# Kernel tuning notes

Hardware: AMD Instinct MI355X
Metric: run time of the kernel (lower is better)

## Reference

```python
import jax, jax.numpy as jnp
import numpy as np

B, L, D = 8, 512, 1024
NUM_SPANS = 6144  # L * max_width


def setup_inputs() -> dict:
    key = jax.random.key(0)
    k_h, k_s, k_w, k_b = jax.random.split(key, 4)
    h = jax.random.normal(k_h, (B, L, D), dtype=jnp.float32)
    span_idx = jax.random.randint(k_s, (B, NUM_SPANS, 2), 0, L, dtype=jnp.int64)
    # Linear(hidden, hidden) params (xavier-ish scale)
    lim = float(np.sqrt(6.0 / (D + D)))
    W = jax.random.uniform(k_w, (D, D), dtype=jnp.float32, minval=-lim, maxval=lim)
    b = jnp.zeros((D,), dtype=jnp.float32)
    return {"h": h, "span_idx": span_idx, "W": W, "b": b}


def reference(h, span_idx, W, b):
    # h: [B, L, D]; span_idx: [B, S, 2] with S = L * width
    Bb, Ll, Dd = h.shape
    start = jnp.clip(span_idx[..., 0], 0, Ll - 1)  # [B, S]
    end = jnp.clip(span_idx[..., 1], 0, Ll - 1)    # [B, S]
    valid = start <= end                            # [B, S]
    # prefix sums: cs[i, t] = sum_{u < t} h[i, u]  -> [B, L+1, D]
    cs = jnp.concatenate([jnp.zeros((Bb, 1, Dd), h.dtype), jnp.cumsum(h, axis=1)], axis=1)
    span_sum = (jnp.take_along_axis(cs, (end + 1)[:, :, None], axis=1)
                - jnp.take_along_axis(cs, start[:, :, None], axis=1))  # [B, S, D]
    count = (end - start + 1).astype(h.dtype)[:, :, None]
    span_rep = jnp.where(valid[:, :, None], span_sum / count, 0.0)  # [B, S, D]
    out = jax.nn.relu(jnp.einsum('bsd,ed->bse', span_rep, W) + b)
    return out.reshape(Bb, Ll, -1, Dd)
```

## Files before the change

### kernel.cpp

```cpp
#include <hip/hip_runtime.h>
#include <hip/hip_bf16.h>
#include <stdint.h>

#define B_DIM 8
#define L_DIM 512
#define D_DIM 1024
#define S_DIM 6144
#define M_DIM (B_DIM * S_DIM)
#define NCHUNK 8
#define CHUNK (L_DIM / NCHUNK)
#define CSB (513 * 1024)

typedef __attribute__((ext_vector_type(8))) short short8;
typedef __attribute__((ext_vector_type(4))) float f32x4;
typedef __attribute__((ext_vector_type(8))) unsigned short us8;

__device__ __forceinline__ unsigned short f2bf(float f) {
    unsigned int u = __float_as_uint(f);
    u += 0x7FFFu + ((u >> 16) & 1u);
    return (unsigned short)(u >> 16);
}

__global__ __launch_bounds__(256) void prep_fused(const float* __restrict__ h,
                                                  float* __restrict__ csum,
                                                  const float* __restrict__ W,
                                                  unsigned short* __restrict__ Wbf) {
    if (blockIdx.x < 256) {
        int tid = blockIdx.x * 256 + threadIdx.x;
        int d = tid & 1023;
        int c = (tid >> 10) & 7;
        int b = tid >> 13;
        const float* hp = h + ((size_t)b * L_DIM + c * CHUNK) * D_DIM + d;
        float s = 0.f;
        #pragma unroll 8
        for (int i = 0; i < CHUNK; ++i) s += hp[(size_t)i * D_DIM];
        csum[tid] = s;
    } else {
        int tid = (blockIdx.x - 256) * 256 + threadIdx.x;
        const float4* p = (const float4*)(W + (size_t)tid * 8);
        float4 a = p[0], c = p[1];
        us8 o;
        o[0] = f2bf(a.x); o[1] = f2bf(a.y); o[2] = f2bf(a.z); o[3] = f2bf(a.w);
        o[4] = f2bf(c.x); o[5] = f2bf(c.y); o[6] = f2bf(c.z); o[7] = f2bf(c.w);
        *(us8*)&Wbf[(size_t)tid * 8] = o;
    }
}

__global__ __launch_bounds__(256) void build_cs(const float* __restrict__ h,
                                                const float* __restrict__ csum,
                                                float* __restrict__ cs) {
    int tid = blockIdx.x * 256 + threadIdx.x;
    int d = tid & 1023;
    int c = (tid >> 10) & 7;
    int b = tid >> 13;
    float p = 0.f;
    for (int cc = 0; cc < c; ++cc)
        p += csum[(b << 13) + (cc << 10) + d];
    const float* hp = h + ((size_t)b * L_DIM + c * CHUNK) * D_DIM + d;
    float* cp = cs + ((size_t)b * (L_DIM + 1) + c * CHUNK) * D_DIM + d;
    if (c == 0) cp[0] = 0.f;
    #pragma unroll 8
    for (int i = 0; i < CHUNK; ++i) {
        p += hp[(size_t)i * D_DIM];
        cp[(size_t)(i + 1) * D_DIM] = p;
    }
}

__global__ __launch_bounds__(256) void spanrep(const float* __restrict__ cs,
                                               const int* __restrict__ span_idx,
                                               unsigned short* __restrict__ rep) {
    int tid = blockIdx.x * 256 + threadIdx.x;
    int d8 = tid & 127;
    int bs = tid >> 7;
    int b = bs / S_DIM;
    int2 se = ((const int2*)span_idx)[bs];
    int st = min(max(se.x, 0), L_DIM - 1);
    int en = min(max(se.y, 0), L_DIM - 1);
    bool valid = st <= en;
    float inv = valid ? 1.0f / (float)(en - st + 1) : 0.0f;
    const float* base = cs + (size_t)b * CSB + d8 * 8;
    const float4* pe = (const float4*)(base + (size_t)(en + 1) * D_DIM);
    const float4* ps = (const float4*)(base + (size_t)st * D_DIM);
    float4 e0 = pe[0], e1 = pe[1];
    float4 s0 = ps[0], s1 = ps[1];
    us8 o;
    o[0] = f2bf((e0.x - s0.x) * inv);
    o[1] = f2bf((e0.y - s0.y) * inv);
    o[2] = f2bf((e0.z - s0.z) * inv);
    o[3] = f2bf((e0.w - s0.w) * inv);
    o[4] = f2bf((e1.x - s1.x) * inv);
    o[5] = f2bf((e1.y - s1.y) * inv);
    o[6] = f2bf((e1.z - s1.z) * inv);
    o[7] = f2bf((e1.w - s1.w) * inv);
    *(us8*)&rep[(size_t)bs * D_DIM + d8 * 8] = o;
}

__global__ __launch_bounds__(512, 2) void gemm_bias_relu(
    const unsigned short* __restrict__ A,
    const unsigned short* __restrict__ Wt,
    const float* __restrict__ bias,
    float* __restrict__ out) {
    constexpr int K = D_DIM, N = D_DIM;
    __shared__ __align__(16) unsigned short As[2][256 * 64];
    __shared__ __align__(16) unsigned short Bs[2][256 * 64];

    const int tid = threadIdx.x;
    const int wid = tid >> 6, lane = tid & 63;

    int blk = blockIdx.x;
    int swz = (blk & 7) * 96 + (blk >> 3);
    const int bm = swz >> 2;
    const int bn = swz & 3;
    const int rowM = bm * 256;
    const int colN = bn * 256;

    const int fr = lane & 15;
    const int kq = lane >> 4;
    const int wr = wid >> 2, wc = wid & 3;

    f32x4 acc[8][4];
    #pragma unroll
    for (int i = 0; i < 8; ++i)
        #pragma unroll
        for (int j = 0; j < 4; ++j) acc[i][j] = (f32x4){0.f, 0.f, 0.f, 0.f};

#define FENCE() do { asm volatile("" ::: "memory"); \
                     __builtin_amdgcn_sched_barrier(0); } while (0)

#define STAGE(k0v, bufi) do { \
        _Pragma("unroll") \
        for (int i = 0; i < 4; ++i) { \
            int ci = i * 512 + tid; \
            int r = ci >> 3, c = ci & 7; \
            int gc = (k0v) + ((c ^ (r & 7)) * 8); \
            const unsigned short* sa = A + (size_t)(rowM + r) * K + gc; \
            __builtin_amdgcn_global_load_lds( \
                (const __attribute__((address_space(1))) void*)sa, \
                (__attribute__((address_space(3))) void*)&As[bufi][(size_t)ci * 8], \
                16, 0, 0); \
            const unsigned short* sb = Wt + (size_t)(colN + r) * K + gc; \
            __builtin_amdgcn_global_load_lds( \
                (const __attribute__((address_space(1))) void*)sb, \
                (__attribute__((address_space(3))) void*)&Bs[bufi][(size_t)ci * 8], \
                16, 0, 0); \
        } \
    } while (0)

#define COMPUTE(bufi) do { \
        _Pragma("unroll") \
        for (int ks = 0; ks < 2; ++ks) { \
            const int kb = ks * 64 + kq * 16; \
            short8 af[8], bq[4]; \
            _Pragma("unroll") \
            for (int i = 0; i < 8; ++i) { \
                int ra = wr * 128 + i * 16 + fr; \
                af[i] = *(const short8*)((const char*)As[bufi] + ra * 128 + (kb ^ ((ra & 7) << 4))); \
            } \
            _Pragma("unroll") \
            for (int j = 0; j < 4; ++j) { \
                int rb = wc * 64 + j * 16 + fr; \
                bq[j] = *(const short8*)((const char*)Bs[bufi] + rb * 128 + (kb ^ ((rb & 7) << 4))); \
            } \
            __builtin_amdgcn_s_setprio(1); \
            _Pragma("unroll") \
            for (int i = 0; i < 8; ++i) \
                _Pragma("unroll") \
                for (int j = 0; j < 4; ++j) \
                    acc[i][j] = __builtin_amdgcn_mfma_f32_16x16x32_bf16(af[i], bq[j], acc[i][j], 0, 0, 0); \
            __builtin_amdgcn_s_setprio(0); \
        } \
    } while (0)

    STAGE(0, 0);
    FENCE();
    asm volatile("s_waitcnt vmcnt(0) lgkmcnt(0)" ::: "memory");
    __builtin_amdgcn_s_barrier();
    FENCE();
    STAGE(64, 1);
    FENCE();

    for (int t = 0; t < 16; ++t) {
        COMPUTE(t & 1);
        if (t < 15) {
            FENCE();
            asm volatile("s_waitcnt vmcnt(0) lgkmcnt(0)" ::: "memory");
            __builtin_amdgcn_s_barrier();
            FENCE();
            if (t < 14) {
                STAGE((t + 2) * 64, t & 1);
                FENCE();
            }
        }
    }

    const int m0 = rowM + wr * 128;
    const int n0 = colN + wc * 64;
    float bv[4];
    #pragma unroll
    for (int j = 0; j < 4; ++j) bv[j] = bias[n0 + j * 16 + fr];
    #pragma unroll
    for (int i = 0; i < 8; ++i)
        #pragma unroll
        for (int j = 0; j < 4; ++j)
            #pragma unroll
            for (int r = 0; r < 4; ++r) {
                int m = m0 + i * 16 + kq * 4 + r;
                int n = n0 + j * 16 + fr;
                float v = acc[i][j][r] + bv[j];
                out[(size_t)m * N + n] = v > 0.f ? v : 0.f;
            }
#undef FENCE
#undef STAGE
#undef COMPUTE
}

extern "C" void kernel_launch(void* const* d_in, const int* in_sizes, int n_in,
                              void* d_out, int out_size, void* d_ws, size_t ws_size,
                              hipStream_t stream) {
    const float* h = (const float*)d_in[0];
    const int* span = (const int*)d_in[1];
    const float* W = (const float*)d_in[2];
    const float* bias = (const float*)d_in[3];
    float* out = (float*)d_out;

    char* ws = (char*)d_ws;
    float* cs = (float*)(ws);
    unsigned short* Wbf = (unsigned short*)(ws + 16809984);
    float* csum = (float*)(ws + 18907136);
    unsigned short* rep = (unsigned short*)(ws + 19169280);

    prep_fused<<<768, 256, 0, stream>>>(h, csum, W, Wbf);
    build_cs<<<256, 256, 0, stream>>>(h, csum, cs);
    spanrep<<<24576, 256, 0, stream>>>(cs, span, rep);
    gemm_bias_relu<<<768, 512, 0, stream>>>(rep, Wbf, bias, out);
}
```

Baseline: 379.6 us.

## Switch GEMM to four-slot K=32 LDS ring with prefetch depth three

```diff
diff --git a/kernel.cpp b/kernel.cpp
--- a/kernel.cpp
+++ b/kernel.cpp
@@ -101,8 +101,8 @@
     const float* __restrict__ bias,
     float* __restrict__ out) {
     constexpr int K = D_DIM, N = D_DIM;
-    __shared__ __align__(16) unsigned short As[2][256 * 64];
-    __shared__ __align__(16) unsigned short Bs[2][256 * 64];
+    __shared__ __align__(16) unsigned short AsL[4 * 8192];
+    __shared__ __align__(16) unsigned short BsL[4 * 8192];
 
     const int tid = threadIdx.x;
     const int wid = tid >> 6, lane = tid & 63;
@@ -118,80 +118,85 @@
     const int kq = lane >> 4;
     const int wr = wid >> 2, wc = wid & 3;
 
+    int aoff[8], boff[4];
+    #pragma unroll
+    for (int i = 0; i < 8; ++i) {
+        int r = wr * 128 + i * 16 + fr;
+        aoff[i] = r * 64 + (((kq ^ (r & 3) ^ ((r >> 2) & 1))) << 4);
+    }
+    #pragma unroll
+    for (int j = 0; j < 4; ++j) {
+        int r = wc * 64 + j * 16 + fr;
+        boff[j] = r * 64 + (((kq ^ (r & 3) ^ ((r >> 2) & 1))) << 4);
+    }
+
     f32x4 acc[8][4];
     #pragma unroll
     for (int i = 0; i < 8; ++i)
         #pragma unroll
         for (int j = 0; j < 4; ++j) acc[i][j] = (f32x4){0.f, 0.f, 0.f, 0.f};
 
-#define FENCE() do { asm volatile("" ::: "memory"); \
-                     __builtin_amdgcn_sched_barrier(0); } while (0)
-
-#define STAGE(k0v, bufi) do { \
-        _Pragma("unroll") \
-        for (int i = 0; i < 4; ++i) { \
-            int ci = i * 512 + tid; \
-            int r = ci >> 3, c = ci & 7; \
-            int gc = (k0v) + ((c ^ (r & 7)) * 8); \
-            const unsigned short* sa = A + (size_t)(rowM + r) * K + gc; \
+#define STAGE(gg) do { \
+        const int kb_ = (gg) * 32; \
+        const int sl_ = ((gg) & 3) * 8192; \
+        _Pragma("unroll") \
+        for (int i_ = 0; i_ < 2; ++i_) { \
+            int ci_ = i_ * 512 + tid; \
+            int r_ = ci_ >> 2, cp_ = ci_ & 3; \
+            int cl_ = cp_ ^ (r_ & 3) ^ ((r_ >> 2) & 1); \
+            const unsigned short* sa_ = A + (size_t)(rowM + r_) * K + kb_ + cl_ * 8; \
             __builtin_amdgcn_global_load_lds( \
-                (const __attribute__((address_space(1))) void*)sa, \
-                (__attribute__((address_space(3))) void*)&As[bufi][(size_t)ci * 8], \
+                (const __attribute__((address_space(1))) void*)sa_, \
+                (__attribute__((address_space(3))) void*)&AsL[sl_ + ci_ * 8], \
                 16, 0, 0); \
-            const unsigned short* sb = Wt + (size_t)(colN + r) * K + gc; \
+            const unsigned short* sb_ = Wt + (size_t)(colN + r_) * K + kb_ + cl_ * 8; \
             __builtin_amdgcn_global_load_lds( \
-                (const __attribute__((address_space(1))) void*)sb, \
-                (__attribute__((address_space(3))) void*)&Bs[bufi][(size_t)ci * 8], \
+                (const __attribute__((address_space(1))) void*)sb_, \
+                (__attribute__((address_space(3))) void*)&BsL[sl_ + ci_ * 8], \
                 16, 0, 0); \
         } \
     } while (0)
 
-#define COMPUTE(bufi) do { \
-        _Pragma("unroll") \
-        for (int ks = 0; ks < 2; ++ks) { \
-            const int kb = ks * 64 + kq * 16; \
-            short8 af[8], bq[4]; \
+#define PHASE(gg, DOSTAGE) do { \
+        short8 af_[8]; short8 bq_[4]; \
+        const char* ab_ = ((const char*)AsL) + ((gg) & 3) * 16384; \
+        const char* bb_ = ((const char*)BsL) + ((gg) & 3) * 16384; \
+        _Pragma("unroll") \
+        for (int i_ = 0; i_ < 8; ++i_) af_[i_] = *(const short8*)(ab_ + aoff[i_]); \
+        _Pragma("unroll") \
+        for (int j_ = 0; j_ < 4; ++j_) bq_[j_] = *(const short8*)(bb_ + boff[j_]); \
+        if (DOSTAGE) STAGE((gg) + 3); \
+        asm volatile("s_waitcnt lgkmcnt(0)" ::: "memory"); \
+        __builtin_amdgcn_sched_barrier(0); \
+        __builtin_amdgcn_s_setprio(1); \
+        _Pragma("unroll") \
+        for (int i_ = 0; i_ < 8; ++i_) \
             _Pragma("unroll") \
-            for (int i = 0; i < 8; ++i) { \
-                int ra = wr * 128 + i * 16 + fr; \
-                af[i] = *(const short8*)((const char*)As[bufi] + ra * 128 + (kb ^ ((ra & 7) << 4))); \
-            } \
-            _Pragma("unroll") \
-            for (int j = 0; j < 4; ++j) { \
-                int rb = wc * 64 + j * 16 + fr; \
-                bq[j] = *(const short8*)((const char*)Bs[bufi] + rb * 128 + (kb ^ ((rb & 7) << 4))); \
-            } \
-            __builtin_amdgcn_s_setprio(1); \
-            _Pragma("unroll") \
-            for (int i = 0; i < 8; ++i) \
-                _Pragma("unroll") \
-                for (int j = 0; j < 4; ++j) \
-                    acc[i][j] = __builtin_amdgcn_mfma_f32_16x16x32_bf16(af[i], bq[j], acc[i][j], 0, 0, 0); \
-            __builtin_amdgcn_s_setprio(0); \
-        } \
+            for (int j_ = 0; j_ < 4; ++j_) \
+                acc[i_][j_] = __builtin_amdgcn_mfma_f32_16x16x32_bf16( \
+                    af_[i_], bq_[j_], acc[i_][j_], 0, 0, 0); \
+        __builtin_amdgcn_s_setprio(0); \
     } while (0)
 
-    STAGE(0, 0);
-    FENCE();
-    asm volatile("s_waitcnt vmcnt(0) lgkmcnt(0)" ::: "memory");
+    STAGE(0);
+    STAGE(1);
+    STAGE(2);
+    asm volatile("s_waitcnt vmcnt(8)" ::: "memory");
     __builtin_amdgcn_s_barrier();
-    FENCE();
-    STAGE(64, 1);
-    FENCE();
-
-    for (int t = 0; t < 16; ++t) {
-        COMPUTE(t & 1);
-        if (t < 15) {
-            FENCE();
-            asm volatile("s_waitcnt vmcnt(0) lgkmcnt(0)" ::: "memory");
-            __builtin_amdgcn_s_barrier();
-            FENCE();
-            if (t < 14) {
-                STAGE((t + 2) * 64, t & 1);
-                FENCE();
-            }
-        }
-    }
+
+    #pragma unroll 4
+    for (int g = 0; g < 29; ++g) {
+        PHASE(g, 1);
+        asm volatile("s_waitcnt vmcnt(8)" ::: "memory");
+        __builtin_amdgcn_s_barrier();
+    }
+    PHASE(29, 0);
+    asm volatile("s_waitcnt vmcnt(4)" ::: "memory");
+    __builtin_amdgcn_s_barrier();
+    PHASE(30, 0);
+    asm volatile("s_waitcnt vmcnt(0)" ::: "memory");
+    __builtin_amdgcn_s_barrier();
+    PHASE(31, 0);
 
     const int m0 = rowM + wr * 128;
     const int n0 = colN + wc * 64;
@@ -209,9 +214,8 @@
                 float v = acc[i][j][r] + bv[j];
                 out[(size_t)m * N + n] = v > 0.f ? v : 0.f;
             }
-#undef FENCE
 #undef STAGE
-#undef COMPUTE
+#undef PHASE
 }
 
 extern "C" void kernel_launch(void* const* d_in, const int* in_sizes, int n_in,
```

New measurement: 373.9 us. No clear change (-1.5%).

## Restructure GEMM main loop into fine-grained interleaved load/compute pipeline

Applied to the files above, without the earlier changes.

```diff
diff --git a/kernel.cpp b/kernel.cpp
--- a/kernel.cpp
+++ b/kernel.cpp
@@ -95,14 +95,14 @@
     *(us8*)&rep[(size_t)bs * D_DIM + d8 * 8] = o;
 }
 
-__global__ __launch_bounds__(512, 2) void gemm_bias_relu(
-    const unsigned short* __restrict__ A,
+__global__ __launch_bounds__(512) void gemm_bias_relu(
+    const unsigned short* __restrict__ Ag,
     const unsigned short* __restrict__ Wt,
     const float* __restrict__ bias,
     float* __restrict__ out) {
     constexpr int K = D_DIM, N = D_DIM;
-    __shared__ __align__(16) unsigned short As[2][256 * 64];
-    __shared__ __align__(16) unsigned short Bs[2][256 * 64];
+    __shared__ __align__(16) unsigned short AsL[2 * 256 * 64];
+    __shared__ __align__(16) unsigned short BsL[2 * 256 * 64];
 
     const int tid = threadIdx.x;
     const int wid = tid >> 6, lane = tid & 63;
@@ -124,74 +124,89 @@
         #pragma unroll
         for (int j = 0; j < 4; ++j) acc[i][j] = (f32x4){0.f, 0.f, 0.f, 0.f};
 
-#define FENCE() do { asm volatile("" ::: "memory"); \
-                     __builtin_amdgcn_sched_barrier(0); } while (0)
-
-#define STAGE(k0v, bufi) do { \
-        _Pragma("unroll") \
-        for (int i = 0; i < 4; ++i) { \
-            int ci = i * 512 + tid; \
-            int r = ci >> 3, c = ci & 7; \
-            int gc = (k0v) + ((c ^ (r & 7)) * 8); \
-            const unsigned short* sa = A + (size_t)(rowM + r) * K + gc; \
+    short8 bq[2][2][4];
+    short8 a3[2][2][4];
+    short8 a7[2][2][4];
+
+#define FEN do { asm volatile("" ::: "memory"); \
+                 __builtin_amdgcn_sched_barrier(0); } while (0)
+#define BARR do { __builtin_amdgcn_s_barrier(); \
+                  __builtin_amdgcn_sched_barrier(0); } while (0)
+#define LGKM0 do { asm volatile("s_waitcnt lgkmcnt(0)" ::: "memory"); \
+                   __builtin_amdgcn_sched_barrier(0); } while (0)
+#define GATE6 do { asm volatile("s_waitcnt vmcnt(6)" ::: "memory"); } while (0)
+#define GATE0 do { asm volatile("s_waitcnt vmcnt(0)" ::: "memory"); } while (0)
+
+#define RD_BQ(P) do { _Pragma("unroll") for (int ks = 0; ks < 2; ++ks) \
+        _Pragma("unroll") for (int j = 0; j < 4; ++j) { \
+            int rb = wc * 64 + j * 16 + fr; \
+            bq[P][ks][j] = *(const short8*)((const char*)BsL + (P) * 32768 \
+                + rb * 128 + ((ks * 64 + kq * 16) ^ ((rb & 7) << 4))); } } while (0)
+
+#define RD_A3(P) do { _Pragma("unroll") for (int ks = 0; ks < 2; ++ks) \
+        _Pragma("unroll") for (int i = 0; i < 4; ++i) { \
+            int ra = wr * 128 + i * 16 + fr; \
+            a3[P][ks][i] = *(const short8*)((const char*)AsL + (P) * 32768 \
+                + ra * 128 + ((ks * 64 + kq * 16) ^ ((ra & 7) << 4))); } } while (0)
+
+#define RD_A7(P) do { _Pragma("unroll") for (int ks = 0; ks < 2; ++ks) \
+        _Pragma("unroll") for (int i = 0; i < 4; ++i) { \
+            int ra = wr * 128 + (i + 4) * 16 + fr; \
+            a7[P][ks][i] = *(const short8*)((const char*)AsL + (P) * 32768 \
+                + ra * 128 + ((ks * 64 + kq * 16) ^ ((ra & 7) << 4))); } } while (0)
+
+#define MM3(P, KS) do { __builtin_amdgcn_s_setprio(1); \
+        _Pragma("unroll") for (int i = 0; i < 4; ++i) \
+        _Pragma("unroll") for (int j = 0; j < 4; ++j) \
+            acc[i][j] = __builtin_amdgcn_mfma_f32_16x16x32_bf16( \
+                a3[P][KS][i], bq[P][KS][j], acc[i][j], 0, 0, 0); \
+        __builtin_amdgcn_s_setprio(0); } while (0)
+
+#define MM7(P, KS) do { __builtin_amdgcn_s_setprio(1); \
+        _Pragma("unroll") for (int i = 0; i < 4; ++i) \
+        _Pragma("unroll") for (int j = 0; j < 4; ++j) \
+            acc[4 + i][j] = __builtin_amdgcn_mfma_f32_16x16x32_bf16( \
+                a7[P][KS][i], bq[P][KS][j], acc[4 + i][j], 0, 0, 0); \
+        __builtin_amdgcn_s_setprio(0); } while (0)
+
+#define STG(tile, ISB, H, BUF) do { const int kb_ = (tile) * 64; \
+        _Pragma("unroll") for (int i2 = 0; i2 < 2; ++i2) { \
+            int ci_ = i2 * 512 + tid; \
+            int r_ = ci_ >> 3, c_ = ci_ & 7; \
+            int gr_ = (H) * 128 + r_; \
+            const unsigned short* s_ = ((ISB) ? Wt + (size_t)(colN + gr_) * K \
+                                              : Ag + (size_t)(rowM + gr_) * K) \
+                                       + kb_ + ((c_ ^ (r_ & 7)) * 8); \
+            unsigned short* d_ = ((ISB) ? BsL : AsL) + (BUF) * 16384 + (size_t)(gr_ * 8 + c_) * 8; \
             __builtin_amdgcn_global_load_lds( \
-                (const __attribute__((address_space(1))) void*)sa, \
-                (__attribute__((address_space(3))) void*)&As[bufi][(size_t)ci * 8], \
-                16, 0, 0); \
-            const unsigned short* sb = Wt + (size_t)(colN + r) * K + gc; \
-            __builtin_amdgcn_global_load_lds( \
-                (const __attribute__((address_space(1))) void*)sb, \
-                (__attribute__((address_space(3))) void*)&Bs[bufi][(size_t)ci * 8], \
-                16, 0, 0); \
-        } \
+                (const __attribute__((address_space(1))) void*)s_, \
+                (__attribute__((address_space(3))) void*)d_, 16, 0, 0); \
+        } } while (0)
+
+#define ITER(T0, FIRST, LAST) do { \
+         RD_BQ(0); STG((T0) + 1, 0, 1, 1); FEN; BARR; LGKM0; \
+                  if (!(FIRST)) MM7(1, 1); FEN; BARR; \
+         RD_A3(0); if (!(LAST)) STG((T0) + 2, 1, 0, 0); FEN; BARR; LGKM0; MM3(0, 0); FEN; BARR; \
+         RD_A7(0); if (!(LAST)) STG((T0) + 2, 1, 1, 0); FEN; BARR; LGKM0; MM7(0, 0); FEN; BARR; \
+         if (!(LAST)) { STG((T0) + 2, 0, 0, 0); FEN; GATE6; } else { GATE0; } \
+                  FEN; BARR; LGKM0; MM3(0, 1); FEN; BARR; \
+         RD_BQ(1); if (!(LAST)) STG((T0) + 2, 0, 1, 0); FEN; BARR; LGKM0; MM7(0, 1); FEN; BARR; \
+         RD_A3(1); if (!(LAST)) STG((T0) + 3, 1, 0, 1); FEN; BARR; LGKM0; MM3(1, 0); FEN; BARR; \
+         RD_A7(1); if (!(LAST)) STG((T0) + 3, 1, 1, 1); FEN; BARR; LGKM0; MM7(1, 0); FEN; BARR; \
+         if (!(LAST)) { STG((T0) + 3, 0, 0, 1); FEN; GATE6; } \
+                  FEN; BARR; LGKM0; MM3(1, 1); FEN; BARR; \
     } while (0)
 
-#define COMPUTE(bufi) do { \
-        _Pragma("unroll") \
-        for (int ks = 0; ks < 2; ++ks) { \
-            const int kb = ks * 64 + kq * 16; \
-            short8 af[8], bq[4]; \
-            _Pragma("unroll") \
-            for (int i = 0; i < 8; ++i) { \
-                int ra = wr * 128 + i * 16 + fr; \
-                af[i] = *(const short8*)((const char*)As[bufi] + ra * 128 + (kb ^ ((ra & 7) << 4))); \
-            } \
-            _Pragma("unroll") \
-            for (int j = 0; j < 4; ++j) { \
-                int rb = wc * 64 + j * 16 + fr; \
-                bq[j] = *(const short8*)((const char*)Bs[bufi] + rb * 128 + (kb ^ ((rb & 7) << 4))); \
-            } \
-            __builtin_amdgcn_s_setprio(1); \
-            _Pragma("unroll") \
-            for (int i = 0; i < 8; ++i) \
-                _Pragma("unroll") \
-                for (int j = 0; j < 4; ++j) \
-                    acc[i][j] = __builtin_amdgcn_mfma_f32_16x16x32_bf16(af[i], bq[j], acc[i][j], 0, 0, 0); \
-            __builtin_amdgcn_s_setprio(0); \
-        } \
-    } while (0)
-
-    STAGE(0, 0);
-    FENCE();
-    asm volatile("s_waitcnt vmcnt(0) lgkmcnt(0)" ::: "memory");
-    __builtin_amdgcn_s_barrier();
-    FENCE();
-    STAGE(64, 1);
-    FENCE();
-
-    for (int t = 0; t < 16; ++t) {
-        COMPUTE(t & 1);
-        if (t < 15) {
-            FENCE();
-            asm volatile("s_waitcnt vmcnt(0) lgkmcnt(0)" ::: "memory");
-            __builtin_amdgcn_s_barrier();
-            FENCE();
-            if (t < 14) {
-                STAGE((t + 2) * 64, t & 1);
-                FENCE();
-            }
-        }
-    }
+    STG(0, 1, 0, 0); STG(0, 1, 1, 0); STG(0, 0, 0, 0); STG(0, 0, 1, 0);
+    STG(1, 1, 0, 1); STG(1, 1, 1, 1); STG(1, 0, 0, 1);
+    FEN;
+    GATE6;
+    BARR;
+
+    ITER(0, 1, 0);
+    for (int T0 = 2; T0 <= 12; T0 += 2) ITER(T0, 0, 0);
+    ITER(14, 0, 1);
+    MM7(1, 1);
 
     const int m0 = rowM + wr * 128;
     const int n0 = colN + wc * 64;
@@ -209,9 +224,18 @@
                 float v = acc[i][j][r] + bv[j];
                 out[(size_t)m * N + n] = v > 0.f ? v : 0.f;
             }
-#undef FENCE
-#undef STAGE
-#undef COMPUTE
+#undef FEN
+#undef BARR
+#undef LGKM0
+#undef GATE6
+#undef GATE0
+#undef RD_BQ
+#undef RD_A3
+#undef RD_A7
+#undef MM3
+#undef MM7
+#undef STG
+#undef ITER
 }
 
 extern "C" void kernel_launch(void* const* d_in, const int* in_sizes, int n_in,
```

Measured after the change: 412.7 us. +8.7%, slower.
